# Optimization experiments

Measured on AMD Instinct MI355X. Metric: run time of the kernel, lower is better.

Reference implementation:

```python
import jax, jax.numpy as jnp
import numpy as np

N = 100000

def gcn_conv(x, src, dst, norm, W, b, num_nodes):
    # x: [N, Cin] -> [N, Cout]; GCNConv: linear transform then normalized sum aggregation
    h = x @ W                                   # [N, Cout]
    msg = h[src] * norm[:, None]                # [E+N, Cout] gather + scale
    out = jax.ops.segment_sum(msg, dst, num_segments=num_nodes)  # scatter-add
    return out + b

def _norm_coeffs(src, dst, num_nodes):
    # symmetric normalization D^{-1/2} A_hat D^{-1/2} with self-loops already in src/dst
    deg = jax.ops.segment_sum(jnp.ones_like(src, dtype=jnp.float32), dst, num_segments=num_nodes)
    dinv = jnp.where(deg > 0, jax.lax.rsqrt(jnp.maximum(deg, 1.0)), 0.0)
    return dinv[src] * dinv[dst]

def setup_inputs() -> dict:
    key = jax.random.key(0)
    ks = jax.random.split(key, 8)
    Cin, Ch, Cout, E = 128, 128, 47, 1600000
    x = jax.random.normal(ks[0], (N, Cin), dtype=jnp.float32)
    edge_index = jax.random.randint(ks[1], (2, E), 0, N, dtype=jnp.int64)
    def glorot(k, fan_in, fan_out):
        s = jnp.sqrt(6.0 / (fan_in + fan_out))
        return jax.random.uniform(k, (fan_in, fan_out), jnp.float32, -s, s)
    return {
        'x': x, 'edge_index': edge_index,
        'W1': glorot(ks[2], Cin, Ch), 'b1': jnp.zeros((Ch,), jnp.float32),
        'W2': glorot(ks[3], Ch, Ch),  'b2': jnp.zeros((Ch,), jnp.float32),
        'W3': glorot(ks[4], Ch, Cout),'b3': jnp.zeros((Cout,), jnp.float32),
    }

def reference(x, edge_index, W1, b1, W2, b2, W3, b3):
    num_nodes = x.shape[0]
    loop = jnp.arange(num_nodes, dtype=edge_index.dtype)
    src = jnp.concatenate([edge_index[0], loop])
    dst = jnp.concatenate([edge_index[1], loop])
    norm = _norm_coeffs(src, dst, num_nodes)
    # eval-mode forward: dropout(p=0.5, training=False) is identity
    h = gcn_conv(x, src, dst, norm, W1, b1, num_nodes)
    h = jax.nn.relu(h)
    h = gcn_conv(h, src, dst, norm, W2, b2, num_nodes)
    h = jax.nn.relu(h)
    h = gcn_conv(h, src, dst, norm, W3, b3, num_nodes)
    return jax.nn.log_softmax(h, axis=1)
```

## Files before the change

### kernel.cpp

```cpp
#include <hip/hip_runtime.h>
#include <stdint.h>

typedef __bf16 bf16x8 __attribute__((ext_vector_type(8)));
typedef float f32x4 __attribute__((ext_vector_type(4)));

#define CHB 8192
#define LDSROW 17

__device__ __forceinline__ unsigned short f2bf(float f) {
    union { float f; unsigned u; } x; x.f = f;
    unsigned r = x.u + 0x7fffu + ((x.u >> 16) & 1u);
    return (unsigned short)(r >> 16);
}

__device__ __forceinline__ void dot2acc(float& a, unsigned pk, unsigned sel) {
    asm("v_dot2_f32_bf16 %0, %1, %2, %0" : "+v"(a) : "v"(pk), "v"(sel));
}

#define SEL_LO 0x00003F80u
#define SEL_HI 0x3F800000u

#define DOT8(v)                                      \
    dot2acc(acc[0], (v).x, sel_lo); dot2acc(acc[1], (v).x, sel_hi); \
    dot2acc(acc[2], (v).y, sel_lo); dot2acc(acc[3], (v).y, sel_hi); \
    dot2acc(acc[4], (v).z, sel_lo); dot2acc(acc[5], (v).z, sel_hi); \
    dot2acc(acc[6], (v).w, sel_lo); dot2acc(acc[7], (v).w, sel_hi);

#define DOT4(v)                                      \
    dot2acc(acc[0], (v).x, sel_lo); dot2acc(acc[1], (v).x, sel_hi); \
    dot2acc(acc[2], (v).y, sel_lo); dot2acc(acc[3], (v).y, sel_hi);

__global__ __launch_bounds__(256) void k_hist(const int* __restrict__ dst, int E, int nPB,
                                              int* __restrict__ bhist, int NB) {
    __shared__ int h[256];
    int t = threadIdx.x;
    h[t] = 0;
    __syncthreads();
    int blk = blockIdx.x;
    int hi = min((blk + 1) * CHB, E);
    for (int e = blk * CHB + t; e < hi; e += 256) atomicAdd(&h[dst[e] >> 9], 1);
    __syncthreads();
    if (t < NB) bhist[t * nPB + blk] = h[t];
}

__global__ __launch_bounds__(256) void k_scan_part(const int* __restrict__ deg,
                                                   int* __restrict__ part, int N) {
    __shared__ int wsum[4];
    int t = threadIdx.x;
    int lane = t & 63, wv = t >> 6;
    int base = blockIdx.x * 1024 + t * 4;
    int s = 0;
#pragma unroll
    for (int j = 0; j < 4; ++j) {
        int i = base + j;
        if (i < N) s += deg[i];
    }
    for (int off = 1; off < 64; off <<= 1) s += __shfl_xor(s, off, 64);
    if (lane == 0) wsum[wv] = s;
    __syncthreads();
    if (t == 0) part[blockIdx.x] = wsum[0] + wsum[1] + wsum[2] + wsum[3];
}

__global__ void k_scan_mid(int* __restrict__ part, int nb) {
    __shared__ int buf[256];
    int t = threadIdx.x;
    buf[t] = (t < nb) ? part[t] : 0;
    __syncthreads();
    for (int off = 1; off < 256; off <<= 1) {
        int v = buf[t];
        int u = (t >= off) ? buf[t - off] : 0;
        __syncthreads();
        buf[t] = v + u;
        __syncthreads();
    }
    if (t < nb) part[t] = (t == 0) ? 0 : buf[t - 1];
}

__global__ __launch_bounds__(256) void k_scan_final(const int* __restrict__ deg,
                                                    const int* __restrict__ part,
                                                    int* __restrict__ out, int N) {
    __shared__ int wsum[4];
    int t = threadIdx.x;
    int lane = t & 63, wv = t >> 6;
    int base = blockIdx.x * 1024 + t * 4;
    int v[4];
    int s = 0;
#pragma unroll
    for (int j = 0; j < 4; ++j) {
        int i = base + j;
        v[j] = (i < N) ? deg[i] : 0;
        s += v[j];
    }
    int inc = s;
    for (int off = 1; off < 64; off <<= 1) {
        int u = __shfl_up(inc, off, 64);
        if (lane >= off) inc += u;
    }
    if (lane == 63) wsum[wv] = inc;
    __syncthreads();
    int excl = part[blockIdx.x] + inc - s;
    for (int w = 0; w < wv; ++w) excl += wsum[w];
#pragma unroll
    for (int j = 0; j < 4; ++j) {
        int i = base + j;
        if (i < N) {
            out[i] = excl;
            excl += v[j];
            if (i == N - 1) out[N] = excl;
        }
    }
}

__global__ __launch_bounds__(256) void k_partition(const int* __restrict__ src,
                                                   const int* __restrict__ dst, int E,
                                                   int nPB, const int* __restrict__ bscan,
                                                   unsigned* __restrict__ part_edges, int NB) {
    __shared__ int cur[256];
    int t = threadIdx.x;
    int blk = blockIdx.x;
    if (t < NB) cur[t] = bscan[t * nPB + blk];
    __syncthreads();
    int hi = min((blk + 1) * CHB, E);
    for (int e = blk * CHB + t; e < hi; e += 256) {
        int d = dst[e];
        int s = src[e];
        int pos = atomicAdd(&cur[d >> 9], 1);
        part_edges[pos] = ((unsigned)(d & 511) << 17) | (unsigned)s;
    }
}

__global__ __launch_bounds__(256) void k_bucket(const unsigned* __restrict__ part_edges,
                                                const int* __restrict__ bscan, int nPB,
                                                int N, int Npad, int* __restrict__ row_ptr,
                                                float* __restrict__ dinv,
                                                int* __restrict__ ssrc) {
    __shared__ int cnt[512];
    __shared__ int excl[512];
    __shared__ int wsum[4];
    int t = threadIdx.x;
    int b = blockIdx.x;
    int pb = bscan[b * nPB];
    int pe = bscan[(b + 1) * nPB];
    cnt[t] = 0; cnt[t + 256] = 0;
    __syncthreads();
    for (int e = pb + t; e < pe; e += 256)
        atomicAdd(&cnt[(part_edges[e] >> 17) & 511], 1);
    __syncthreads();
    int a0 = cnt[2 * t], a1 = cnt[2 * t + 1];
    int s = a0 + a1;
    int lane = t & 63, wv = t >> 6;
    int inc = s;
    for (int off = 1; off < 64; off <<= 1) {
        int u = __shfl_up(inc, off, 64);
        if (lane >= off) inc += u;
    }
    if (lane == 63) wsum[wv] = inc;
    __syncthreads();
    int pre = inc - s;
    for (int w = 0; w < wv; ++w) pre += wsum[w];
    excl[2 * t] = pre;
    excl[2 * t + 1] = pre + a0;
    int base = b << 9;
#pragma unroll
    for (int j = 0; j < 2; ++j) {
        int i = 2 * t + j;
        int g = base + i;
        int c = (j == 0) ? a0 : a1;
        int ex = (j == 0) ? pre : pre + a0;
        if (g < N) {
            row_ptr[g] = pb + ex;
            if (g == N - 1) row_ptr[N] = pb + ex + c;
        }
        if (g < Npad) dinv[g] = rsqrtf((float)c + 1.0f);
    }
    __syncthreads();
    for (int e = pb + t; e < pe; e += 256) {
        unsigned pk = part_edges[e];
        int doff = (pk >> 17) & 511;
        int pos = pb + atomicAdd(&excl[doff], 1);
        ssrc[pos] = (int)(pk & 0x1FFFFu);
    }
}

__global__ void k_wfrag(const float* __restrict__ W, unsigned short* __restrict__ Wf,
                        int Ncol, int realCols) {
    int NT = Ncol >> 4;
    int total = 4 * NT * 64 * 8;
    int idx = blockIdx.x * blockDim.x + threadIdx.x;
    if (idx >= total) return;
    int j = idx & 7;
    int l = (idx >> 3) & 63;
    int t = idx >> 9;
    int n = t % NT;
    int kk = t / NT;
    int k = kk * 32 + ((l >> 4) << 3) + j;
    int c = (n << 4) + (l & 15);
    float v = (c < realCols) ? W[k * realCols + c] : 0.0f;
    Wf[idx] = f2bf(v);
}

__global__ __launch_bounds__(256) void k_gemm_f32(const float* __restrict__ X,
                                                  const unsigned short* __restrict__ Wf,
                                                  const float* __restrict__ dinv,
                                                  unsigned short* __restrict__ Hout, int N) {
    int lane = threadIdx.x & 63;
    int wv = threadIdx.x >> 6;
    size_t row0 = (size_t)(blockIdx.x * 4 + wv) * 16;
    int arowi = (int)row0 + (lane & 15);
    const float* arow = X + (size_t)arowi * 128 + ((lane >> 4) << 3);
    bool vr = arowi < N;
    f32x4 acc[8];
#pragma unroll
    for (int n = 0; n < 8; ++n) acc[n] = (f32x4){0.f, 0.f, 0.f, 0.f};
#pragma unroll
    for (int kk = 0; kk < 4; ++kk) {
        union { bf16x8 v; unsigned short u[8]; } A;
        if (vr) {
            float4 f0 = *(const float4*)(arow + kk * 32);
            float4 f1 = *(const float4*)(arow + kk * 32 + 4);
            A.u[0] = f2bf(f0.x); A.u[1] = f2bf(f0.y);
            A.u[2] = f2bf(f0.z); A.u[3] = f2bf(f0.w);
            A.u[4] = f2bf(f1.x); A.u[5] = f2bf(f1.y);
            A.u[6] = f2bf(f1.z); A.u[7] = f2bf(f1.w);
        } else {
#pragma unroll
            for (int j = 0; j < 8; ++j) A.u[j] = 0;
        }
#pragma unroll
        for (int n = 0; n < 8; ++n) {
            bf16x8 b = *(const bf16x8*)(Wf + (((kk * 8 + n) * 64 + lane) << 3));
            acc[n] = __builtin_amdgcn_mfma_f32_16x16x32_bf16(A.v, b, acc[n], 0, 0, 0);
        }
    }
    size_t crow = row0 + ((lane >> 4) << 2);
    int ccol = lane & 15;
    float dv[4];
#pragma unroll
    for (int q = 0; q < 4; ++q) dv[q] = dinv[crow + q];
#pragma unroll
    for (int n = 0; n < 8; ++n) {
#pragma unroll
        for (int q = 0; q < 4; ++q) {
            Hout[(crow + q) * 128 + n * 16 + ccol] = f2bf(acc[n][q] * dv[q]);
        }
    }
}

template<int NT>
__global__ __launch_bounds__(256) void k_agg_gemm(const unsigned short* __restrict__ H,
                                                  const int* __restrict__ row_ptr,
                                                  const int* __restrict__ ssrc,
                                                  const float* __restrict__ dinv,
                                                  const float* __restrict__ bias,
                                                  const unsigned short* __restrict__ Wf,
                                                  unsigned short* __restrict__ Hout, int N) {
    __shared__ uint4 lds[64 * LDSROW];
    int lane = threadIdx.x & 63;
    int wv = threadIdx.x >> 6;
    int g = lane >> 4;
    int c16 = lane & 15;
    unsigned sel_lo = SEL_LO, sel_hi = SEL_HI;
    const uint4* Hv = (const uint4*)H;
    const int iBase = blockIdx.x * 64 + wv * 16;

    for (int ii = 0; ii < 16; ++ii) {
        int i = iBase + ii;
        float acc[8];
#pragma unroll
        for (int c = 0; c < 8; ++c) acc[c] = 0.f;
        if (i < N) {
            if (g == 0) {
                uint4 v = Hv[((size_t)i << 4) + c16];
                DOT8(v);
            }
            int e0 = row_ptr[i], e1 = row_ptr[i + 1];
            for (int base = e0; base < e1; base += 64) {
                int cnt = min(64, e1 - base);
                int sidx = (lane < cnt) ? ssrc[base + lane] : 0;
                int full = cnt & ~3;
#pragma unroll 4
                for (int j = 0; j < full; j += 4) {
                    int s = __shfl(sidx, j + g, 64);
                    uint4 v = Hv[((size_t)s << 4) + c16];
                    DOT8(v);
                }
                int jj = full + g;
                if (jj < cnt) {
                    int s = __shfl(sidx, jj, 64);
                    uint4 v = Hv[((size_t)s << 4) + c16];
                    DOT8(v);
                }
            }
        }
#pragma unroll
        for (int c = 0; c < 8; ++c) {
            acc[c] += __shfl_xor(acc[c], 16, 64);
            acc[c] += __shfl_xor(acc[c], 32, 64);
        }
        if (g == 0) {
            float dv = dinv[i];
            const float4* bv = (const float4*)bias;
            float4 b0 = bv[c16 * 2], b1 = bv[c16 * 2 + 1];
            float r0 = fmaxf(acc[0] * dv + b0.x, 0.f);
            float r1 = fmaxf(acc[1] * dv + b0.y, 0.f);
            float r2 = fmaxf(acc[2] * dv + b0.z, 0.f);
            float r3 = fmaxf(acc[3] * dv + b0.w, 0.f);
            float r4 = fmaxf(acc[4] * dv + b1.x, 0.f);
            float r5 = fmaxf(acc[5] * dv + b1.y, 0.f);
            float r6 = fmaxf(acc[6] * dv + b1.z, 0.f);
            float r7 = fmaxf(acc[7] * dv + b1.w, 0.f);
            uint4 o;
            o.x = (unsigned)f2bf(r0) | ((unsigned)f2bf(r1) << 16);
            o.y = (unsigned)f2bf(r2) | ((unsigned)f2bf(r3) << 16);
            o.z = (unsigned)f2bf(r4) | ((unsigned)f2bf(r5) << 16);
            o.w = (unsigned)f2bf(r6) | ((unsigned)f2bf(r7) << 16);
            lds[(wv * 16 + ii) * LDSROW + c16] = o;
        }
    }
    __syncthreads();

    f32x4 gacc[NT];
#pragma unroll
    for (int n = 0; n < NT; ++n) gacc[n] = (f32x4){0.f, 0.f, 0.f, 0.f};
    const uint4* arow = &lds[(wv * 16 + (lane & 15)) * LDSROW];
#pragma unroll
    for (int kk = 0; kk < 4; ++kk) {
        union { bf16x8 v; uint4 q; } A;
        A.q = arow[kk * 4 + (lane >> 4)];
#pragma unroll
        for (int n = 0; n < NT; ++n) {
            bf16x8 b = *(const bf16x8*)(Wf + (((kk * NT + n) * 64 + lane) << 3));
            gacc[n] = __builtin_amdgcn_mfma_f32_16x16x32_bf16(A.v, b, gacc[n], 0, 0, 0);
        }
    }
    const int NCOL = NT * 16;
    size_t row0 = (size_t)iBase;
    size_t crow = row0 + ((lane >> 4) << 2);
    int ccol = lane & 15;
    float dv[4];
#pragma unroll
    for (int q = 0; q < 4; ++q) dv[q] = dinv[crow + q];
#pragma unroll
    for (int n = 0; n < NT; ++n) {
#pragma unroll
        for (int q = 0; q < 4; ++q) {
            Hout[(crow + q) * NCOL + n * 16 + ccol] = f2bf(gacc[n][q] * dv[q]);
        }
    }
}

__global__ __launch_bounds__(256) void k_agg3(const unsigned short* __restrict__ H,
                                              const int* __restrict__ row_ptr,
                                              const int* __restrict__ ssrc,
                                              const float* __restrict__ dinv,
                                              const float* __restrict__ b3,
                                              float* __restrict__ Out, int N, int Cout) {
    int lane = threadIdx.x & 63;
    int i = blockIdx.x * 4 + (threadIdx.x >> 6);
    if (i >= N) return;
    unsigned sel_lo = SEL_LO, sel_hi = SEL_HI;
    int g = lane >> 4;
    int c16 = lane & 15;
    const uint2* Hv = (const uint2*)H;
    float acc[4];
#pragma unroll
    for (int c = 0; c < 4; ++c) acc[c] = 0.f;
    int e0 = row_ptr[i], e1 = row_ptr[i + 1];
    for (int base = e0; base < e1; base += 64) {
        int cnt = min(64, e1 - base);
        int sidx = (lane < cnt) ? ssrc[base + lane] : 0;
        int full = cnt & ~3;
#pragma unroll 4
        for (int j = 0; j < full; j += 4) {
            int s = __shfl(sidx, j + g, 64);
            uint2 v = Hv[((size_t)s << 4) + c16];
            DOT4(v);
        }
        int jj = full + g;
        if (jj < cnt) {
            int s = __shfl(sidx, jj, 64);
            uint2 v = Hv[((size_t)s << 4) + c16];
            DOT4(v);
        }
    }
    if (g == 0) {
        uint2 v = Hv[((size_t)i << 4) + c16];
        DOT4(v);
    }
#pragma unroll
    for (int c = 0; c < 4; ++c) {
        acc[c] += __shfl_xor(acc[c], 16, 64);
        acc[c] += __shfl_xor(acc[c], 32, 64);
    }
    float t0 = __shfl(acc[0], lane >> 2, 64);
    float t1 = __shfl(acc[1], lane >> 2, 64);
    float t2 = __shfl(acc[2], lane >> 2, 64);
    float t3 = __shfl(acc[3], lane >> 2, 64);
    float a01 = (lane & 1) ? t1 : t0;
    float a23 = (lane & 1) ? t3 : t2;
    float av  = (lane & 2) ? a23 : a01;
    float dv = dinv[i];
    float z = (lane < Cout) ? av * dv + b3[lane] : -1e30f;
    float m = z;
    for (int off = 32; off; off >>= 1) m = fmaxf(m, __shfl_xor(m, off, 64));
    float pexp = (lane < Cout) ? expf(z - m) : 0.f;
    float ssum = pexp;
    for (int off = 32; off; off >>= 1) ssum += __shfl_xor(ssum, off, 64);
    if (lane < Cout) Out[(size_t)i * Cout + lane] = z - m - logf(ssum);
}

extern "C" void kernel_launch(void* const* d_in, const int* in_sizes, int n_in,
                              void* d_out, int out_size, void* d_ws, size_t ws_size,
                              hipStream_t stream) {
    const float* x  = (const float*)d_in[0];
    const int*   ei = (const int*)d_in[1];
    const float* W1 = (const float*)d_in[2];
    const float* b1 = (const float*)d_in[3];
    const float* W2 = (const float*)d_in[4];
    const float* b2 = (const float*)d_in[5];
    const float* W3 = (const float*)d_in[6];
    const float* b3 = (const float*)d_in[7];

    const int N = in_sizes[0] / 128;
    const int E = in_sizes[1] / 2;
    const int Cout = in_sizes[7];
    const int Npad = (N + 63) & ~63;
    const int* srcp = ei;
    const int* dstp = ei + E;

    const int NB  = (N + 511) >> 9;
    const int nPB = (E + CHB - 1) / CHB;
    const int M   = NB * nPB;

    char* p = (char*)d_ws;
    auto alloc = [&](size_t bytes) -> void* {
        void* r = (void*)p;
        p += (bytes + 255) & ~(size_t)255;
        return r;
    };
    float* dinv     = (float*)alloc((size_t)Npad * 4);
    int*   row_ptr  = (int*)alloc((size_t)(N + 1) * 4);
    int*   bhist    = (int*)alloc((size_t)M * 4);
    int*   bscan    = (int*)alloc((size_t)(M + 1) * 4);
    int*   part     = (int*)alloc(1024 * 4);
    unsigned* pedge = (unsigned*)alloc((size_t)E * 4);
    int*   ssrc     = (int*)alloc((size_t)E * 4);
    unsigned short* hb  = (unsigned short*)alloc((size_t)Npad * 128 * 2);
    unsigned short* ab  = (unsigned short*)alloc((size_t)Npad * 128 * 2);
    unsigned short* wf1 = (unsigned short*)alloc(128 * 128 * 2);
    unsigned short* wf2 = (unsigned short*)alloc(128 * 128 * 2);
    unsigned short* wf3 = (unsigned short*)alloc(128 * 64 * 2);

    const int nb2 = (M + 1023) / 1024;
    k_hist<<<nPB, 256, 0, stream>>>(dstp, E, nPB, bhist, NB);
    k_scan_part<<<nb2, 256, 0, stream>>>(bhist, part, M);
    k_scan_mid<<<1, 256, 0, stream>>>(part, nb2);
    k_scan_final<<<nb2, 256, 0, stream>>>(bhist, part, bscan, M);
    k_partition<<<nPB, 256, 0, stream>>>(srcp, dstp, E, nPB, bscan, pedge, NB);
    k_bucket<<<NB, 256, 0, stream>>>(pedge, bscan, nPB, N, Npad, row_ptr, dinv, ssrc);

    k_wfrag<<<(16384 + 255) / 256, 256, 0, stream>>>(W1, wf1, 128, 128);
    k_wfrag<<<(16384 + 255) / 256, 256, 0, stream>>>(W2, wf2, 128, 128);
    k_wfrag<<<(8192 + 255) / 256, 256, 0, stream>>>(W3, wf3, 64, Cout);

    const int gemmGrid = Npad / 64;
    const int aggGrid = (N + 3) / 4;

    k_gemm_f32<<<gemmGrid, 256, 0, stream>>>(x, wf1, dinv, hb, N);
    k_agg_gemm<8><<<gemmGrid, 256, 0, stream>>>(hb, row_ptr, ssrc, dinv, b1, wf2, ab, N);
    k_agg_gemm<4><<<gemmGrid, 256, 0, stream>>>(ab, row_ptr, ssrc, dinv, b2, wf3, hb, N);
    k_agg3<<<aggGrid, 256, 0, stream>>>(hb, row_ptr, ssrc, dinv, b3,
                                        (float*)d_out, N, Cout);
}
```

Baseline: 324.9 us.

## Split fused aggregate+GEMM kernels into separate per-node aggregation and GEMM kernels

Replaces the fused k_agg_gemm kernel, where each wave aggregated 16 nodes one after another and then ran an MFMA GEMM from LDS, with a standalone aggregation kernel (one wave per node) followed by a standalone bf16 GEMM kernel. The aim is much finer-grained parallelism and better load balance in the gather-heavy aggregation, which was serialized per wave. The cost is an extra round trip of the intermediate activations through global memory and two extra launches. The three weight-fragment kernels are also merged into one launch.

```diff
diff --git a/kernel.cpp b/kernel.cpp
--- a/kernel.cpp
+++ b/kernel.cpp
@@ -5,7 +5,6 @@
 typedef float f32x4 __attribute__((ext_vector_type(4)));
 
 #define CHB 8192
-#define LDSROW 17
 
 __device__ __forceinline__ unsigned short f2bf(float f) {
     union { float f; unsigned u; } x; x.f = f;
@@ -182,12 +181,8 @@
     }
 }
 
-__global__ void k_wfrag(const float* __restrict__ W, unsigned short* __restrict__ Wf,
-                        int Ncol, int realCols) {
-    int NT = Ncol >> 4;
-    int total = 4 * NT * 64 * 8;
-    int idx = blockIdx.x * blockDim.x + threadIdx.x;
-    if (idx >= total) return;
+__device__ __forceinline__ void wfrag_one(const float* W, unsigned short* Wf, int idx,
+                                          int NT, int realCols) {
     int j = idx & 7;
     int l = (idx >> 3) & 63;
     int t = idx >> 9;
@@ -197,6 +192,17 @@
     int c = (n << 4) + (l & 15);
     float v = (c < realCols) ? W[k * realCols + c] : 0.0f;
     Wf[idx] = f2bf(v);
+}
+
+__global__ void k_wfrag_all(const float* __restrict__ W1, const float* __restrict__ W2,
+                            const float* __restrict__ W3,
+                            unsigned short* __restrict__ wf1,
+                            unsigned short* __restrict__ wf2,
+                            unsigned short* __restrict__ wf3, int Cout) {
+    int idx = blockIdx.x * blockDim.x + threadIdx.x;
+    if (idx < 16384) wfrag_one(W1, wf1, idx, 8, 128);
+    else if (idx < 32768) wfrag_one(W2, wf2, idx - 16384, 8, 128);
+    else if (idx < 40960) wfrag_one(W3, wf3, idx - 32768, 4, Cout);
 }
 
 __global__ __launch_bounds__(256) void k_gemm_f32(const float* __restrict__ X,
@@ -247,94 +253,28 @@
 }
 
 template<int NT>
-__global__ __launch_bounds__(256) void k_agg_gemm(const unsigned short* __restrict__ H,
-                                                  const int* __restrict__ row_ptr,
-                                                  const int* __restrict__ ssrc,
-                                                  const float* __restrict__ dinv,
-                                                  const float* __restrict__ bias,
-                                                  const unsigned short* __restrict__ Wf,
-                                                  unsigned short* __restrict__ Hout, int N) {
-    __shared__ uint4 lds[64 * LDSROW];
+__global__ __launch_bounds__(256) void k_gemm(const unsigned short* __restrict__ A,
+                                              const unsigned short* __restrict__ Wf,
+                                              const float* __restrict__ dinv,
+                                              unsigned short* __restrict__ Hout) {
     int lane = threadIdx.x & 63;
     int wv = threadIdx.x >> 6;
-    int g = lane >> 4;
-    int c16 = lane & 15;
-    unsigned sel_lo = SEL_LO, sel_hi = SEL_HI;
-    const uint4* Hv = (const uint4*)H;
-    const int iBase = blockIdx.x * 64 + wv * 16;
-
-    for (int ii = 0; ii < 16; ++ii) {
-        int i = iBase + ii;
-        float acc[8];
-#pragma unroll
-        for (int c = 0; c < 8; ++c) acc[c] = 0.f;
-        if (i < N) {
-            if (g == 0) {
-                uint4 v = Hv[((size_t)i << 4) + c16];
-                DOT8(v);
-            }
-            int e0 = row_ptr[i], e1 = row_ptr[i + 1];
-            for (int base = e0; base < e1; base += 64) {
-                int cnt = min(64, e1 - base);
-                int sidx = (lane < cnt) ? ssrc[base + lane] : 0;
-                int full = cnt & ~3;
-#pragma unroll 4
-                for (int j = 0; j < full; j += 4) {
-                    int s = __shfl(sidx, j + g, 64);
-                    uint4 v = Hv[((size_t)s << 4) + c16];
-                    DOT8(v);
-                }
-                int jj = full + g;
-                if (jj < cnt) {
-                    int s = __shfl(sidx, jj, 64);
-                    uint4 v = Hv[((size_t)s << 4) + c16];
-                    DOT8(v);
-                }
-            }
-        }
-#pragma unroll
-        for (int c = 0; c < 8; ++c) {
-            acc[c] += __shfl_xor(acc[c], 16, 64);
-            acc[c] += __shfl_xor(acc[c], 32, 64);
-        }
-        if (g == 0) {
-            float dv = dinv[i];
-            const float4* bv = (const float4*)bias;
-            float4 b0 = bv[c16 * 2], b1 = bv[c16 * 2 + 1];
-            float r0 = fmaxf(acc[0] * dv + b0.x, 0.f);
-            float r1 = fmaxf(acc[1] * dv + b0.y, 0.f);
-            float r2 = fmaxf(acc[2] * dv + b0.z, 0.f);
-            float r3 = fmaxf(acc[3] * dv + b0.w, 0.f);
-            float r4 = fmaxf(acc[4] * dv + b1.x, 0.f);
-            float r5 = fmaxf(acc[5] * dv + b1.y, 0.f);
-            float r6 = fmaxf(acc[6] * dv + b1.z, 0.f);
-            float r7 = fmaxf(acc[7] * dv + b1.w, 0.f);
-            uint4 o;
-            o.x = (unsigned)f2bf(r0) | ((unsigned)f2bf(r1) << 16);
-            o.y = (unsigned)f2bf(r2) | ((unsigned)f2bf(r3) << 16);
-            o.z = (unsigned)f2bf(r4) | ((unsigned)f2bf(r5) << 16);
-            o.w = (unsigned)f2bf(r6) | ((unsigned)f2bf(r7) << 16);
-            lds[(wv * 16 + ii) * LDSROW + c16] = o;
-        }
-    }
-    __syncthreads();
-
-    f32x4 gacc[NT];
-#pragma unroll
-    for (int n = 0; n < NT; ++n) gacc[n] = (f32x4){0.f, 0.f, 0.f, 0.f};
-    const uint4* arow = &lds[(wv * 16 + (lane & 15)) * LDSROW];
+    int rb = blockIdx.x * 4 + wv;
+    size_t row0 = (size_t)rb * 16;
+    const unsigned short* arow = A + (row0 + (lane & 15)) * 128 + ((lane >> 4) << 3);
+    f32x4 acc[NT];
+#pragma unroll
+    for (int n = 0; n < NT; ++n) acc[n] = (f32x4){0.f, 0.f, 0.f, 0.f};
 #pragma unroll
     for (int kk = 0; kk < 4; ++kk) {
-        union { bf16x8 v; uint4 q; } A;
-        A.q = arow[kk * 4 + (lane >> 4)];
+        bf16x8 a = *(const bf16x8*)(arow + kk * 32);
 #pragma unroll
         for (int n = 0; n < NT; ++n) {
             bf16x8 b = *(const bf16x8*)(Wf + (((kk * NT + n) * 64 + lane) << 3));
-            gacc[n] = __builtin_amdgcn_mfma_f32_16x16x32_bf16(A.v, b, gacc[n], 0, 0, 0);
+            acc[n] = __builtin_amdgcn_mfma_f32_16x16x32_bf16(a, b, acc[n], 0, 0, 0);
         }
     }
     const int NCOL = NT * 16;
-    size_t row0 = (size_t)iBase;
     size_t crow = row0 + ((lane >> 4) << 2);
     int ccol = lane & 15;
     float dv[4];
@@ -344,8 +284,72 @@
     for (int n = 0; n < NT; ++n) {
 #pragma unroll
         for (int q = 0; q < 4; ++q) {
-            Hout[(crow + q) * NCOL + n * 16 + ccol] = f2bf(gacc[n][q] * dv[q]);
-        }
+            Hout[(crow + q) * NCOL + n * 16 + ccol] = f2bf(acc[n][q] * dv[q]);
+        }
+    }
+}
+
+__global__ __launch_bounds__(256) void k_agg(const unsigned short* __restrict__ H,
+                                             const int* __restrict__ row_ptr,
+                                             const int* __restrict__ ssrc,
+                                             const float* __restrict__ dinv,
+                                             const float* __restrict__ bias,
+                                             unsigned short* __restrict__ Out, int N) {
+    int lane = threadIdx.x & 63;
+    int i = blockIdx.x * 4 + (threadIdx.x >> 6);
+    if (i >= N) return;
+    unsigned sel_lo = SEL_LO, sel_hi = SEL_HI;
+    int g = lane >> 4;
+    int c16 = lane & 15;
+    const uint4* Hv = (const uint4*)H;
+    float acc[8];
+#pragma unroll
+    for (int c = 0; c < 8; ++c) acc[c] = 0.f;
+    int e0 = row_ptr[i], e1 = row_ptr[i + 1];
+    for (int base = e0; base < e1; base += 64) {
+        int cnt = min(64, e1 - base);
+        int sidx = (lane < cnt) ? ssrc[base + lane] : 0;
+        int full = cnt & ~3;
+#pragma unroll 4
+        for (int j = 0; j < full; j += 4) {
+            int s = __shfl(sidx, j + g, 64);
+            uint4 v = Hv[((size_t)s << 4) + c16];
+            DOT8(v);
+        }
+        int jj = full + g;
+        if (jj < cnt) {
+            int s = __shfl(sidx, jj, 64);
+            uint4 v = Hv[((size_t)s << 4) + c16];
+            DOT8(v);
+        }
+    }
+    if (g == 0) {
+        uint4 v = Hv[((size_t)i << 4) + c16];
+        DOT8(v);
+    }
+#pragma unroll
+    for (int c = 0; c < 8; ++c) {
+        acc[c] += __shfl_xor(acc[c], 16, 64);
+        acc[c] += __shfl_xor(acc[c], 32, 64);
+    }
+    if (g == 0) {
+        float dv = dinv[i];
+        const float4* bv = (const float4*)bias;
+        float4 b0 = bv[c16 * 2], b1 = bv[c16 * 2 + 1];
+        float r0 = fmaxf(acc[0] * dv + b0.x, 0.f);
+        float r1 = fmaxf(acc[1] * dv + b0.y, 0.f);
+        float r2 = fmaxf(acc[2] * dv + b0.z, 0.f);
+        float r3 = fmaxf(acc[3] * dv + b0.w, 0.f);
+        float r4 = fmaxf(acc[4] * dv + b1.x, 0.f);
+        float r5 = fmaxf(acc[5] * dv + b1.y, 0.f);
+        float r6 = fmaxf(acc[6] * dv + b1.z, 0.f);
+        float r7 = fmaxf(acc[7] * dv + b1.w, 0.f);
+        uint4 o;
+        o.x = (unsigned)f2bf(r0) | ((unsigned)f2bf(r1) << 16);
+        o.y = (unsigned)f2bf(r2) | ((unsigned)f2bf(r3) << 16);
+        o.z = (unsigned)f2bf(r4) | ((unsigned)f2bf(r5) << 16);
+        o.w = (unsigned)f2bf(r6) | ((unsigned)f2bf(r7) << 16);
+        ((uint4*)Out)[((size_t)i << 4) + c16] = o;
     }
 }
 
@@ -459,16 +463,16 @@
     k_partition<<<nPB, 256, 0, stream>>>(srcp, dstp, E, nPB, bscan, pedge, NB);
     k_bucket<<<NB, 256, 0, stream>>>(pedge, bscan, nPB, N, Npad, row_ptr, dinv, ssrc);
 
-    k_wfrag<<<(16384 + 255) / 256, 256, 0, stream>>>(W1, wf1, 128, 128);
-    k_wfrag<<<(16384 + 255) / 256, 256, 0, stream>>>(W2, wf2, 128, 128);
-    k_wfrag<<<(8192 + 255) / 256, 256, 0, stream>>>(W3, wf3, 64, Cout);
+    k_wfrag_all<<<160, 256, 0, stream>>>(W1, W2, W3, wf1, wf2, wf3, Cout);
 
     const int gemmGrid = Npad / 64;
     const int aggGrid = (N + 3) / 4;
 
     k_gemm_f32<<<gemmGrid, 256, 0, stream>>>(x, wf1, dinv, hb, N);
-    k_agg_gemm<8><<<gemmGrid, 256, 0, stream>>>(hb, row_ptr, ssrc, dinv, b1, wf2, ab, N);
-    k_agg_gemm<4><<<gemmGrid, 256, 0, stream>>>(ab, row_ptr, ssrc, dinv, b2, wf3, hb, N);
+    k_agg<<<aggGrid, 256, 0, stream>>>(hb, row_ptr, ssrc, dinv, b1, ab, N);
+    k_gemm<8><<<gemmGrid, 256, 0, stream>>>(ab, wf2, dinv, hb);
+    k_agg<<<aggGrid, 256, 0, stream>>>(hb, row_ptr, ssrc, dinv, b2, ab, N);
+    k_gemm<4><<<gemmGrid, 256, 0, stream>>>(ab, wf3, dinv, hb);
     k_agg3<<<aggGrid, 256, 0, stream>>>(hb, row_ptr, ssrc, dinv, b3,
                                         (float*)d_out, N, Cout);
 }
```

Result: faster. 292.9 us, median of 2 (-9.9%).
